# Performance work log

Hardware: AMD Instinct MI355X
Metric: run time of the kernel (lower is better)

## Reference

```python
import jax, jax.numpy as jnp
import numpy as np

EPS = 1e-12  # torch F.normalize default eps


def setup_inputs() -> dict:
    key = jax.random.key(0)
    k1, k2, k3, k4 = jax.random.split(key, 4)
    B, M, D = 4, 8192, 512
    N, P = 128, 1
    x = jax.random.normal(k1, (B, M, D), dtype=jnp.float32)
    phi = jax.random.normal(k2, (D, N, P), dtype=jnp.float32) * (1.0 / D ** 0.5)
    scale = jnp.ones((1,), dtype=jnp.float32)
    W = jax.random.normal(k3, (N, D, D), dtype=jnp.float32) * (1.0 / D ** 0.5)
    b = jax.random.normal(k4, (N, D), dtype=jnp.float32) * 0.01
    return {"x": x, "phi": phi, "scale": scale, "W": W, "b": b}


def _l2norm(v, axis):
    return v / jnp.maximum(jnp.linalg.norm(v, axis=axis, keepdims=True), EPS)


def reference(x, phi, scale, W, b):
    # normalize tokens along feature dim, phi along dim axis, scale phi
    xn = _l2norm(x, axis=2)                      # [B,M,D]
    phin = scale * _l2norm(phi, axis=0)          # [D,N,P]
    logits = jnp.einsum('bmd,dnp->bmnp', xn, phin)
    B, M, N, P = logits.shape
    d = jax.nn.softmax(logits, axis=1)           # dispatch weights (over tokens)
    c = jax.nn.softmax(logits.reshape(B, M, N * P), axis=-1).reshape(B, M, N, P)  # combine (over slots)
    xs = jnp.einsum('bmd,bmnp->bnpd', xn, d)     # slot inputs [B,N,P,D]
    # per-expert Linear, batched over experts (grouped GEMM)
    ys = jnp.einsum('bnpd,nde->bnpe', xs, W) + b[None, :, None, :]
    y = jnp.einsum('bnpd,bmnp->bmd', ys, c)
    return y
```

## Files before the change

### kernel.cpp

```cpp
#include <hip/hip_runtime.h>
#include <math.h>

#define B_ 4
#define M_ 8192
#define D_ 512
#define N_ 128
#define TOK (B_ * M_)
#define MC_ 16
#define MLEN (M_ / MC_)

#define OFF_CS 0
#define OFF_PBT (OFF_CS + 512)
#define OFF_EBN (OFF_PBT + N_ * D_ / 2)
#define OFF_EWT (OFF_EBN + (size_t)TOK * N_ / 2)
#define OFF_XBT (OFF_EWT + (size_t)N_ * TOK / 2)
#define OFF_YST (OFF_XBT + (size_t)D_ * TOK / 2)
#define OFF_XP (OFF_YST + B_ * D_ * N_ / 2)

typedef __attribute__((ext_vector_type(8))) short s16x8;
typedef __attribute__((ext_vector_type(4))) float f32x4;

__device__ inline short f2bf(float f) {
    union { float f; unsigned u; } v;
    v.f = f;
    unsigned r = v.u + 0x7fffu + ((v.u >> 16) & 1u);
    return (short)(r >> 16);
}

__global__ __launch_bounds__(128) void k_phinorm(const float* __restrict__ phi,
                                                 const float* __restrict__ scale,
                                                 short* __restrict__ pbt) {
    __shared__ float sred[128];
    int n = blockIdx.x, tid = threadIdx.x;
    float ss = 0.f;
    for (int d = tid; d < D_; d += 128) {
        float v = phi[d * N_ + n];
        ss += v * v;
    }
    sred[tid] = ss;
    __syncthreads();
    for (int s = 64; s > 0; s >>= 1) {
        if (tid < s) sred[tid] += sred[tid + s];
        __syncthreads();
    }
    float sc = scale[0] / fmaxf(sqrtf(sred[0]), 1e-12f);
    for (int d = tid; d < D_; d += 128) pbt[n * D_ + d] = f2bf(phi[d * N_ + n] * sc);
}

__global__ __launch_bounds__(512) void k_logits(const float* __restrict__ x,
                                                const short* __restrict__ pbt,
                                                short* __restrict__ ebn,
                                                short* __restrict__ ewt,
                                                short* __restrict__ xbt,
                                                float* __restrict__ colsum) {
    __shared__ short smem[4 * 128 * 40];
    __shared__ float rnS[128];
    __shared__ float rsH[2][128];

    int t = threadIdx.x;
    int r0 = blockIdx.x * 128;
    int sm = t >> 2;
    int kq = (t & 3) * 8;
    const float* xrow = &x[(size_t)(r0 + sm) * D_ + kq];
    const short* brow = &pbt[sm * D_ + kq];
    int wid = t >> 6, lane = t & 63;
    int quad = lane >> 4, l15 = lane & 15;
    int mw = (wid >> 1) * 32, nw = (wid & 1) * 64;
    int dl = t & 31, mg = t >> 5;
    f32x4 acc[2][4] = {};
    float ss = 0.f;

    {
        float4 a0 = *(const float4*)&xrow[0];
        float4 a1 = *(const float4*)&xrow[4];
        s16x8 bv = *(const s16x8*)&brow[0];
        ss += a0.x * a0.x + a0.y * a0.y + a0.z * a0.z + a0.w * a0.w +
              a1.x * a1.x + a1.y * a1.y + a1.z * a1.z + a1.w * a1.w;
        s16x8 av;
        av[0] = f2bf(a0.x); av[1] = f2bf(a0.y); av[2] = f2bf(a0.z); av[3] = f2bf(a0.w);
        av[4] = f2bf(a1.x); av[5] = f2bf(a1.y); av[6] = f2bf(a1.z); av[7] = f2bf(a1.w);
        *(s16x8*)&smem[0 * 5120 + sm * 40 + kq] = av;
        *(s16x8*)&smem[10240 + 0 * 5120 + sm * 40 + kq] = bv;
    }
    __syncthreads();

#pragma unroll
    for (int kt = 0; kt < 16; kt++) {
        int cur = kt & 1;
        short* As = &smem[cur * 5120];
        short* Bs = &smem[10240 + cur * 5120];
        float4 na0, na1;
        s16x8 nbv;
        if (kt < 15) {
            na0 = *(const float4*)&xrow[(kt + 1) * 32];
            na1 = *(const float4*)&xrow[(kt + 1) * 32 + 4];
            nbv = *(const s16x8*)&brow[(kt + 1) * 32];
        }
        s16x8 af[2], bfr[4];
#pragma unroll
        for (int i = 0; i < 2; i++)
            af[i] = *(const s16x8*)&As[(mw + i * 16 + l15) * 40 + quad * 8];
#pragma unroll
        for (int j = 0; j < 4; j++)
            bfr[j] = *(const s16x8*)&Bs[(nw + j * 16 + l15) * 40 + quad * 8];
#pragma unroll
        for (int i = 0; i < 2; i++)
#pragma unroll
            for (int j = 0; j < 4; j++)
                acc[i][j] = __builtin_amdgcn_mfma_f32_16x16x32_bf16(af[i], bfr[j], acc[i][j], 0, 0, 0);
        {
            s16x8 tv;
#pragma unroll
            for (int r = 0; r < 8; r++) tv[r] = As[(mg * 8 + r) * 40 + dl];
            *(s16x8*)&xbt[(size_t)(kt * 32 + dl) * TOK + r0 + mg * 8] = tv;
        }
        if (kt < 15) {
            ss += na0.x * na0.x + na0.y * na0.y + na0.z * na0.z + na0.w * na0.w +
                  na1.x * na1.x + na1.y * na1.y + na1.z * na1.z + na1.w * na1.w;
            s16x8 nav;
            nav[0] = f2bf(na0.x); nav[1] = f2bf(na0.y); nav[2] = f2bf(na0.z); nav[3] = f2bf(na0.w);
            nav[4] = f2bf(na1.x); nav[5] = f2bf(na1.y); nav[6] = f2bf(na1.z); nav[7] = f2bf(na1.w);
            *(s16x8*)&smem[(cur ^ 1) * 5120 + sm * 40 + kq] = nav;
            *(s16x8*)&smem[10240 + (cur ^ 1) * 5120 + sm * 40 + kq] = nbv;
        }
        __syncthreads();
    }
    ss += __shfl_xor(ss, 1, 64);
    ss += __shfl_xor(ss, 2, 64);
    if ((t & 3) == 0) rnS[sm] = 1.0f / fmaxf(sqrtf(ss), 1e-12f);
    __syncthreads();

    int bb = r0 >> 13;
    float rv[2][4];
#pragma unroll
    for (int i = 0; i < 2; i++) {
        int ml = mw + i * 16 + quad * 4;
        rv[i][0] = rnS[ml]; rv[i][1] = rnS[ml + 1];
        rv[i][2] = rnS[ml + 2]; rv[i][3] = rnS[ml + 3];
    }
    float rs[2][4] = {};
    short4 ebf[2][4];
#pragma unroll
    for (int j = 0; j < 4; j++) {
        int n = nw + j * 16 + l15;
        float cs = 0.f;
#pragma unroll
        for (int i = 0; i < 2; i++) {
            f32x4 vv = acc[i][j];
            float e0 = __expf(vv[0] * rv[i][0]), e1 = __expf(vv[1] * rv[i][1]);
            float e2 = __expf(vv[2] * rv[i][2]), e3 = __expf(vv[3] * rv[i][3]);
            acc[i][j][0] = e0; acc[i][j][1] = e1; acc[i][j][2] = e2; acc[i][j][3] = e3;
            cs += e0 + e1 + e2 + e3;
            rs[i][0] += e0; rs[i][1] += e1; rs[i][2] += e2; rs[i][3] += e3;
            short4 eb = {f2bf(e0 * rv[i][0]), f2bf(e1 * rv[i][1]),
                         f2bf(e2 * rv[i][2]), f2bf(e3 * rv[i][3])};
            ebf[i][j] = eb;
        }
        cs += __shfl_xor(cs, 16, 64);
        cs += __shfl_xor(cs, 32, 64);
        if (lane < 16) atomicAdd(&colsum[bb * N_ + n], cs);
    }
#pragma unroll
    for (int off = 1; off <= 8; off <<= 1)
#pragma unroll
        for (int i = 0; i < 2; i++)
#pragma unroll
            for (int r = 0; r < 4; r++) rs[i][r] += __shfl_xor(rs[i][r], off, 64);
    if (l15 == 0) {
#pragma unroll
        for (int i = 0; i < 2; i++)
#pragma unroll
            for (int r = 0; r < 4; r++)
                rsH[wid & 1][mw + i * 16 + quad * 4 + r] = rs[i][r];
    }
    __syncthreads();
    float ri[2][4];
#pragma unroll
    for (int i = 0; i < 2; i++)
#pragma unroll
        for (int r = 0; r < 4; r++) {
            int m = mw + i * 16 + quad * 4 + r;
            ri[i][r] = 1.0f / (rsH[0][m] + rsH[1][m]);
        }

    short* T = smem;
#pragma unroll
    for (int h = 0; h < 2; h++) {
        if ((wid & 1) == h) {
#pragma unroll
            for (int i = 0; i < 2; i++) {
                int mb = mw + i * 16 + quad * 4;
#pragma unroll
                for (int j = 0; j < 4; j++) {
                    int nl = j * 16 + l15;
                    *(short4*)&T[nl * 136 + mb] = ebf[i][j];
                }
            }
        }
        __syncthreads();
        {
            int nl = t >> 3, c = t & 7;
            s16x8 v0 = *(const s16x8*)&T[nl * 136 + c * 16];
            s16x8 v1 = *(const s16x8*)&T[nl * 136 + c * 16 + 8];
            size_t go = (size_t)(h * 64 + nl) * TOK + r0 + c * 16;
            *(s16x8*)&ewt[go] = v0;
            *(s16x8*)&ewt[go + 8] = v1;
        }
        __syncthreads();
    }

    short* T2 = smem;
#pragma unroll
    for (int j = 0; j < 4; j++) {
        int n = nw + j * 16 + l15;
#pragma unroll
        for (int i = 0; i < 2; i++) {
            int m = mw + i * 16 + quad * 4;
            f32x4 vv = acc[i][j];
            T2[(m + 0) * 136 + n] = f2bf(vv[0] * ri[i][0]);
            T2[(m + 1) * 136 + n] = f2bf(vv[1] * ri[i][1]);
            T2[(m + 2) * 136 + n] = f2bf(vv[2] * ri[i][2]);
            T2[(m + 3) * 136 + n] = f2bf(vv[3] * ri[i][3]);
        }
    }
    __syncthreads();
    {
        int row = t >> 2, c = (t & 3) * 32;
        s16x8 v0 = *(const s16x8*)&T2[row * 136 + c];
        s16x8 v1 = *(const s16x8*)&T2[row * 136 + c + 8];
        s16x8 v2 = *(const s16x8*)&T2[row * 136 + c + 16];
        s16x8 v3 = *(const s16x8*)&T2[row * 136 + c + 24];
        size_t go = (size_t)(r0 + row) * N_ + c;
        *(s16x8*)&ebn[go] = v0;
        *(s16x8*)&ebn[go + 8] = v1;
        *(s16x8*)&ebn[go + 16] = v2;
        *(s16x8*)&ebn[go + 24] = v3;
    }
}

__global__ __launch_bounds__(512) void k_xs(const short* __restrict__ ewt,
                                            const short* __restrict__ xbt,
                                            float* __restrict__ part) {
    __shared__ short An[2][128 * 40];
    __shared__ short Bd[2][128 * 40];
    int t = threadIdx.x;
    int bid = blockIdx.x;
    int bi = (bid & 7) * 32 + (bid >> 3);
    int dt = bi & 3, mc = (bi >> 2) & 15, b = bi >> 6;
    int d0 = dt * 128;
    size_t mbase = (size_t)b * M_ + (size_t)mc * MLEN;
    int rs = t >> 2, kq = (t & 3) * 8;
    const short* arow = &ewt[(size_t)rs * TOK + mbase + kq];
    const short* brow = &xbt[(size_t)(d0 + rs) * TOK + mbase + kq];
    int wid = t >> 6, lane = t & 63;
    int quad = lane >> 4, l15 = lane & 15;
    int nw = (wid >> 2) * 64, dw = (wid & 3) * 32;
    f32x4 acc[4][2] = {};

    {
        s16x8 ra = *(const s16x8*)&arow[0];
        s16x8 rb = *(const s16x8*)&brow[0];
        *(s16x8*)&An[0][rs * 40 + kq] = ra;
        *(s16x8*)&Bd[0][rs * 40 + kq] = rb;
    }
    __syncthreads();

#pragma unroll
    for (int kt = 0; kt < 16; kt++) {
        int cur = kt & 1;
        s16x8 ra, rb;
        if (kt < 15) {
            ra = *(const s16x8*)&arow[(kt + 1) * 32];
            rb = *(const s16x8*)&brow[(kt + 1) * 32];
        }
        s16x8 af[4], bf[2];
#pragma unroll
        for (int i = 0; i < 4; i++)
            af[i] = *(const s16x8*)&An[cur][(nw + i * 16 + l15) * 40 + quad * 8];
#pragma unroll
        for (int j = 0; j < 2; j++)
            bf[j] = *(const s16x8*)&Bd[cur][(dw + j * 16 + l15) * 40 + quad * 8];
#pragma unroll
        for (int i = 0; i < 4; i++)
#pragma unroll
            for (int j = 0; j < 2; j++)
                acc[i][j] = __builtin_amdgcn_mfma_f32_16x16x32_bf16(af[i], bf[j], acc[i][j], 0, 0, 0);
        if (kt < 15) {
            *(s16x8*)&An[cur ^ 1][rs * 40 + kq] = ra;
            *(s16x8*)&Bd[cur ^ 1][rs * 40 + kq] = rb;
        }
        __syncthreads();
    }
    size_t pbase = (((size_t)mc * B_ + b) * N_) * D_ + d0;
#pragma unroll
    for (int i = 0; i < 4; i++) {
        int nb = nw + i * 16 + quad * 4;
#pragma unroll
        for (int j = 0; j < 2; j++) {
            int d = dw + j * 16 + l15;
            f32x4 vv = acc[i][j];
            part[pbase + (size_t)(nb + 0) * D_ + d] = vv[0];
            part[pbase + (size_t)(nb + 1) * D_ + d] = vv[1];
            part[pbase + (size_t)(nb + 2) * D_ + d] = vv[2];
            part[pbase + (size_t)(nb + 3) * D_ + d] = vv[3];
        }
    }
}

__global__ __launch_bounds__(256) void k_ys(const float* __restrict__ part,
                                            const float* __restrict__ colsum,
                                            const float* __restrict__ W,
                                            const float* __restrict__ bias,
                                            short* __restrict__ ysT) {
    __shared__ float xsn[B_][D_];
    int bi = blockIdx.x;
    int n = bi >> 2, eq = bi & 3;
    int tid = threadIdx.x;
    {
        int lb = tid >> 6, ld = (tid & 63) * 8;
        float inv = 1.0f / colsum[lb * N_ + n];
        float s0 = 0, s1 = 0, s2 = 0, s3 = 0, s4 = 0, s5 = 0, s6 = 0, s7 = 0;
#pragma unroll
        for (int mc = 0; mc < MC_; mc++) {
            const float* p = &part[(((size_t)mc * B_ + lb) * N_ + n) * D_ + ld];
            float4 v0 = *(const float4*)p;
            float4 v1 = *(const float4*)(p + 4);
            s0 += v0.x; s1 += v0.y; s2 += v0.z; s3 += v0.w;
            s4 += v1.x; s5 += v1.y; s6 += v1.z; s7 += v1.w;
        }
        float4 o0 = {s0 * inv, s1 * inv, s2 * inv, s3 * inv};
        float4 o1 = {s4 * inv, s5 * inv, s6 * inv, s7 * inv};
        *(float4*)&xsn[lb][ld] = o0;
        *(float4*)&xsn[lb][ld + 4] = o1;
    }
    __syncthreads();
    int b = tid >> 6;
    int lane = tid & 63;
    int dh = lane >> 5, l32 = lane & 31;
    int e = eq * 128 + l32 * 4;
    const float* Wn = W + (size_t)n * D_ * D_ + e;
    float a0 = 0.f, a1 = 0.f, a2 = 0.f, a3 = 0.f;
    int dbase = dh * 256;
#pragma unroll 8
    for (int d = dbase; d < dbase + 256; d++) {
        float4 w = *(const float4*)&Wn[(size_t)d * D_];
        float xv = xsn[b][d];
        a0 += xv * w.x;
        a1 += xv * w.y;
        a2 += xv * w.z;
        a3 += xv * w.w;
    }
    a0 += __shfl_xor(a0, 32, 64);
    a1 += __shfl_xor(a1, 32, 64);
    a2 += __shfl_xor(a2, 32, 64);
    a3 += __shfl_xor(a3, 32, 64);
    if (dh == 0) {
        float4 bv = *(const float4*)&bias[n * D_ + e];
        ysT[((size_t)b * D_ + e + 0) * N_ + n] = f2bf(a0 + bv.x);
        ysT[((size_t)b * D_ + e + 1) * N_ + n] = f2bf(a1 + bv.y);
        ysT[((size_t)b * D_ + e + 2) * N_ + n] = f2bf(a2 + bv.z);
        ysT[((size_t)b * D_ + e + 3) * N_ + n] = f2bf(a3 + bv.w);
    }
}

__global__ __launch_bounds__(256) void k_combine(const short* __restrict__ ebn,
                                                 const short* __restrict__ ysT,
                                                 float* __restrict__ y) {
    __shared__ short As[128 * 40];
    __shared__ short Bs[128 * 40];
    int t = threadIdx.x;
    int bid = blockIdx.x;
    int bi = (bid & 7) * 128 + (bid >> 3);
    int dt = bi & 3, mt = bi >> 2;
    int r0 = mt * 128, d0 = dt * 128;
    int bb = r0 >> 13;
    int sm = t >> 1, nh = (t & 1) * 16;
    const short* erow = &ebn[(size_t)(r0 + sm) * N_ + nh];
    const short* yrow = &ysT[((size_t)bb * D_ + d0 + sm) * N_ + nh];
    int wid = t >> 6, lane = t & 63;
    int quad = lane >> 4, l15 = lane & 15;
    int mw = (wid >> 1) * 64, dw = (wid & 1) * 64;
    f32x4 acc[4][4] = {};

#pragma unroll
    for (int ks = 0; ks < 4; ks++) {
        int n0 = ks * 32;
        s16x8 ev0 = *(const s16x8*)&erow[n0];
        s16x8 ev1 = *(const s16x8*)&erow[n0 + 8];
        s16x8 yv0 = *(const s16x8*)&yrow[n0];
        s16x8 yv1 = *(const s16x8*)&yrow[n0 + 8];
        *(s16x8*)&As[sm * 40 + nh] = ev0;
        *(s16x8*)&As[sm * 40 + nh + 8] = ev1;
        *(s16x8*)&Bs[sm * 40 + nh] = yv0;
        *(s16x8*)&Bs[sm * 40 + nh + 8] = yv1;
        __syncthreads();
        s16x8 af[4], bf[4];
#pragma unroll
        for (int i = 0; i < 4; i++)
            af[i] = *(const s16x8*)&As[(mw + i * 16 + l15) * 40 + quad * 8];
#pragma unroll
        for (int j = 0; j < 4; j++)
            bf[j] = *(const s16x8*)&Bs[(dw + j * 16 + l15) * 40 + quad * 8];
#pragma unroll
        for (int i = 0; i < 4; i++)
#pragma unroll
            for (int j = 0; j < 4; j++)
                acc[i][j] = __builtin_amdgcn_mfma_f32_16x16x32_bf16(af[i], bf[j], acc[i][j], 0, 0, 0);
        __syncthreads();
    }
#pragma unroll
    for (int i = 0; i < 4; i++) {
        int mb = mw + i * 16 + quad * 4;
#pragma unroll
        for (int j = 0; j < 4; j++) {
            int d = d0 + dw + j * 16 + l15;
            f32x4 v = acc[i][j];
            y[(size_t)(r0 + mb + 0) * D_ + d] = v[0];
            y[(size_t)(r0 + mb + 1) * D_ + d] = v[1];
            y[(size_t)(r0 + mb + 2) * D_ + d] = v[2];
            y[(size_t)(r0 + mb + 3) * D_ + d] = v[3];
        }
    }
}

extern "C" void kernel_launch(void* const* d_in, const int* in_sizes, int n_in,
                              void* d_out, int out_size, void* d_ws, size_t ws_size,
                              hipStream_t stream) {
    const float* x = (const float*)d_in[0];
    const float* phi = (const float*)d_in[1];
    const float* scale = (const float*)d_in[2];
    const float* W = (const float*)d_in[3];
    const float* bias = (const float*)d_in[4];
    float* y = (float*)d_out;
    float* ws = (float*)d_ws;

    float* colsum = ws + OFF_CS;
    short* pbt = (short*)(ws + OFF_PBT);
    short* ebn = (short*)(ws + OFF_EBN);
    short* ewt = (short*)(ws + OFF_EWT);
    short* xbt = (short*)(ws + OFF_XBT);
    short* ysT = (short*)(ws + OFF_YST);
    float* part = ws + OFF_XP;

    hipMemsetAsync(colsum, 0, 512 * sizeof(float), stream);

    k_phinorm<<<N_, 128, 0, stream>>>(phi, scale, pbt);
    k_logits<<<TOK / 128, 512, 0, stream>>>(x, pbt, ebn, ewt, xbt, colsum);
    k_xs<<<B_ * MC_ * 4, 512, 0, stream>>>(ewt, xbt, part);
    k_ys<<<N_ * 4, 256, 0, stream>>>(part, colsum, W, bias, ysT);
    k_combine<<<(TOK / 128) * 4, 256, 0, stream>>>(ebn, ysT, y);
}
```

Before: 311.0 us.

## Reuse W loads across batches in k_ys and use packed bf16 conversion

The k_ys expert GEMV is restructured so each thread accumulates all four batches from a single W load, instead of each wave reading W for one batch. This cuts W global traffic by about four times. Partial sums are combined through a shared-memory reduction, and block indices are swizzled across expert groups. Separately, the manual fp32-to-bf16 rounding in the logits kernel is replaced with the hardware v_cvt_pk_bf16_f32 packed conversion, which lowers VALU instruction count.

```diff
diff --git a/kernel.cpp b/kernel.cpp
--- a/kernel.cpp
+++ b/kernel.cpp
@@ -25,6 +25,12 @@
     v.f = f;
     unsigned r = v.u + 0x7fffu + ((v.u >> 16) & 1u);
     return (short)(r >> 16);
+}
+
+__device__ inline unsigned cvtpk(float a, float b) {
+    unsigned d;
+    asm("v_cvt_pk_bf16_f32 %0, %1, %2" : "=v"(d) : "v"(a), "v"(b));
+    return d;
 }
 
 __global__ __launch_bounds__(128) void k_phinorm(const float* __restrict__ phi,
@@ -76,10 +82,10 @@
         s16x8 bv = *(const s16x8*)&brow[0];
         ss += a0.x * a0.x + a0.y * a0.y + a0.z * a0.z + a0.w * a0.w +
               a1.x * a1.x + a1.y * a1.y + a1.z * a1.z + a1.w * a1.w;
-        s16x8 av;
-        av[0] = f2bf(a0.x); av[1] = f2bf(a0.y); av[2] = f2bf(a0.z); av[3] = f2bf(a0.w);
-        av[4] = f2bf(a1.x); av[5] = f2bf(a1.y); av[6] = f2bf(a1.z); av[7] = f2bf(a1.w);
-        *(s16x8*)&smem[0 * 5120 + sm * 40 + kq] = av;
+        uint4 av;
+        av.x = cvtpk(a0.x, a0.y); av.y = cvtpk(a0.z, a0.w);
+        av.z = cvtpk(a1.x, a1.y); av.w = cvtpk(a1.z, a1.w);
+        *(uint4*)&smem[0 * 5120 + sm * 40 + kq] = av;
         *(s16x8*)&smem[10240 + 0 * 5120 + sm * 40 + kq] = bv;
     }
     __syncthreads();
@@ -117,10 +123,10 @@
         if (kt < 15) {
             ss += na0.x * na0.x + na0.y * na0.y + na0.z * na0.z + na0.w * na0.w +
                   na1.x * na1.x + na1.y * na1.y + na1.z * na1.z + na1.w * na1.w;
-            s16x8 nav;
-            nav[0] = f2bf(na0.x); nav[1] = f2bf(na0.y); nav[2] = f2bf(na0.z); nav[3] = f2bf(na0.w);
-            nav[4] = f2bf(na1.x); nav[5] = f2bf(na1.y); nav[6] = f2bf(na1.z); nav[7] = f2bf(na1.w);
-            *(s16x8*)&smem[(cur ^ 1) * 5120 + sm * 40 + kq] = nav;
+            uint4 nav;
+            nav.x = cvtpk(na0.x, na0.y); nav.y = cvtpk(na0.z, na0.w);
+            nav.z = cvtpk(na1.x, na1.y); nav.w = cvtpk(na1.z, na1.w);
+            *(uint4*)&smem[(cur ^ 1) * 5120 + sm * 40 + kq] = nav;
             *(s16x8*)&smem[10240 + (cur ^ 1) * 5120 + sm * 40 + kq] = nbv;
         }
         __syncthreads();
@@ -139,7 +145,7 @@
         rv[i][2] = rnS[ml + 2]; rv[i][3] = rnS[ml + 3];
     }
     float rs[2][4] = {};
-    short4 ebf[2][4];
+    uint2 ebf[2][4];
 #pragma unroll
     for (int j = 0; j < 4; j++) {
         int n = nw + j * 16 + l15;
@@ -152,9 +158,8 @@
             acc[i][j][0] = e0; acc[i][j][1] = e1; acc[i][j][2] = e2; acc[i][j][3] = e3;
             cs += e0 + e1 + e2 + e3;
             rs[i][0] += e0; rs[i][1] += e1; rs[i][2] += e2; rs[i][3] += e3;
-            short4 eb = {f2bf(e0 * rv[i][0]), f2bf(e1 * rv[i][1]),
-                         f2bf(e2 * rv[i][2]), f2bf(e3 * rv[i][3])};
-            ebf[i][j] = eb;
+            ebf[i][j].x = cvtpk(e0 * rv[i][0], e1 * rv[i][1]);
+            ebf[i][j].y = cvtpk(e2 * rv[i][2], e3 * rv[i][3]);
         }
         cs += __shfl_xor(cs, 16, 64);
         cs += __shfl_xor(cs, 32, 64);
@@ -193,7 +198,7 @@
 #pragma unroll
                 for (int j = 0; j < 4; j++) {
                     int nl = j * 16 + l15;
-                    *(short4*)&T[nl * 136 + mb] = ebf[i][j];
+                    *(uint2*)&T[nl * 136 + mb] = ebf[i][j];
                 }
             }
         }
@@ -217,10 +222,12 @@
         for (int i = 0; i < 2; i++) {
             int m = mw + i * 16 + quad * 4;
             f32x4 vv = acc[i][j];
-            T2[(m + 0) * 136 + n] = f2bf(vv[0] * ri[i][0]);
-            T2[(m + 1) * 136 + n] = f2bf(vv[1] * ri[i][1]);
-            T2[(m + 2) * 136 + n] = f2bf(vv[2] * ri[i][2]);
-            T2[(m + 3) * 136 + n] = f2bf(vv[3] * ri[i][3]);
+            unsigned w01 = cvtpk(vv[0] * ri[i][0], vv[1] * ri[i][1]);
+            unsigned w23 = cvtpk(vv[2] * ri[i][2], vv[3] * ri[i][3]);
+            T2[(m + 0) * 136 + n] = (short)(w01 & 0xffffu);
+            T2[(m + 1) * 136 + n] = (short)(w01 >> 16);
+            T2[(m + 2) * 136 + n] = (short)(w23 & 0xffffu);
+            T2[(m + 3) * 136 + n] = (short)(w23 >> 16);
         }
     }
     __syncthreads();
@@ -313,7 +320,9 @@
                                             const float* __restrict__ bias,
                                             short* __restrict__ ysT) {
     __shared__ float xsn[B_][D_];
-    int bi = blockIdx.x;
+    __shared__ float red[4][32][17];
+    int bid = blockIdx.x;
+    int bi = (bid & 7) * 64 + (bid >> 3);
     int n = bi >> 2, eq = bi & 3;
     int tid = threadIdx.x;
     {
@@ -334,32 +343,57 @@
         *(float4*)&xsn[lb][ld + 4] = o1;
     }
     __syncthreads();
-    int b = tid >> 6;
-    int lane = tid & 63;
-    int dh = lane >> 5, l32 = lane & 31;
+    int l32 = tid & 31, dh = tid >> 5;
     int e = eq * 128 + l32 * 4;
     const float* Wn = W + (size_t)n * D_ * D_ + e;
-    float a0 = 0.f, a1 = 0.f, a2 = 0.f, a3 = 0.f;
-    int dbase = dh * 256;
-#pragma unroll 8
-    for (int d = dbase; d < dbase + 256; d++) {
-        float4 w = *(const float4*)&Wn[(size_t)d * D_];
-        float xv = xsn[b][d];
-        a0 += xv * w.x;
-        a1 += xv * w.y;
-        a2 += xv * w.z;
-        a3 += xv * w.w;
-    }
-    a0 += __shfl_xor(a0, 32, 64);
-    a1 += __shfl_xor(a1, 32, 64);
-    a2 += __shfl_xor(a2, 32, 64);
-    a3 += __shfl_xor(a3, 32, 64);
-    if (dh == 0) {
-        float4 bv = *(const float4*)&bias[n * D_ + e];
-        ysT[((size_t)b * D_ + e + 0) * N_ + n] = f2bf(a0 + bv.x);
-        ysT[((size_t)b * D_ + e + 1) * N_ + n] = f2bf(a1 + bv.y);
-        ysT[((size_t)b * D_ + e + 2) * N_ + n] = f2bf(a2 + bv.z);
-        ysT[((size_t)b * D_ + e + 3) * N_ + n] = f2bf(a3 + bv.w);
+    float a[4][4] = {};
+    int dbase = dh * 64;
+#pragma unroll 2
+    for (int dc = 0; dc < 64; dc += 4) {
+        int d = dbase + dc;
+        f32x4 xv[4];
+#pragma unroll
+        for (int b = 0; b < 4; b++) xv[b] = *(const f32x4*)&xsn[b][d];
+#pragma unroll
+        for (int u = 0; u < 4; u++) {
+            float4 w = *(const float4*)&Wn[(size_t)(d + u) * D_];
+#pragma unroll
+            for (int b = 0; b < 4; b++) {
+                a[b][0] += xv[b][u] * w.x;
+                a[b][1] += xv[b][u] * w.y;
+                a[b][2] += xv[b][u] * w.z;
+                a[b][3] += xv[b][u] * w.w;
+            }
+        }
+    }
+#pragma unroll
+    for (int b = 0; b < 4; b++)
+#pragma unroll
+        for (int c = 0; c < 4; c++) a[b][c] += __shfl_xor(a[b][c], 32, 64);
+    int wv = tid >> 6, lane = tid & 63;
+    if (lane < 32) {
+#pragma unroll
+        for (int b = 0; b < 4; b++)
+#pragma unroll
+            for (int c = 0; c < 4; c++) red[wv][lane][b * 4 + c] = a[b][c];
+    }
+    __syncthreads();
+    if (tid < 128) {
+        int b = tid >> 5, l = tid & 31;
+        float r0 = 0, r1 = 0, r2 = 0, r3 = 0;
+#pragma unroll
+        for (int w = 0; w < 4; w++) {
+            r0 += red[w][l][b * 4 + 0];
+            r1 += red[w][l][b * 4 + 1];
+            r2 += red[w][l][b * 4 + 2];
+            r3 += red[w][l][b * 4 + 3];
+        }
+        int ee = eq * 128 + l * 4;
+        float4 bv = *(const float4*)&bias[n * D_ + ee];
+        ysT[((size_t)b * D_ + ee + 0) * N_ + n] = f2bf(r0 + bv.x);
+        ysT[((size_t)b * D_ + ee + 1) * N_ + n] = f2bf(r1 + bv.y);
+        ysT[((size_t)b * D_ + ee + 2) * N_ + n] = f2bf(r2 + bv.z);
+        ysT[((size_t)b * D_ + ee + 3) * N_ + n] = f2bf(r3 + bv.w);
     }
 }
 
```

Measured after the change: 309.2 us. Within noise of the previous version (-0.6%).
